# Optimization experiments

Hardware: AMD Instinct MI355X
Metric: run time of the kernel (lower is better)

The kernel has to match this reference:

```python
import jax, jax.numpy as jnp
import numpy as np

LN_EPS = 1e-5

def _layer_norm(x, gamma, beta):
    mu = jnp.mean(x, axis=-1, keepdims=True)
    var = jnp.mean(jnp.square(x - mu), axis=-1, keepdims=True)
    return (x - mu) * jax.lax.rsqrt(var + LN_EPS) * gamma + beta

def setup_inputs() -> dict:
    key = jax.random.key(0)
    ks = jax.random.split(key, 6)
    B, Lc, S, H = 8, 16384, 2048, 256
    char_embeddings = jax.random.normal(ks[0], (B, Lc, H), dtype=jnp.float32)
    # include some negative indices (-1, -2) to exercise the no-token mask path
    token_alignment = jax.random.randint(ks[1], (B, Lc), -2, S, dtype=jnp.int32).astype(jnp.int64)
    decoder_hidden_states = jax.random.normal(ks[2], (B, S, H), dtype=jnp.float32)
    scale1 = 1.0 / np.sqrt(2 * H)
    W1 = jax.random.normal(ks[3], (2 * H, H), dtype=jnp.float32) * scale1
    b1 = jnp.zeros((H,), dtype=jnp.float32)
    W2 = jax.random.normal(ks[4], (2 * H, H), dtype=jnp.float32) * scale1
    b2 = jnp.zeros((H,), dtype=jnp.float32)
    ln_gamma = jnp.ones((H,), dtype=jnp.float32)
    ln_beta = jnp.zeros((H,), dtype=jnp.float32)
    return {
        "char_embeddings": char_embeddings,
        "token_alignment": token_alignment,
        "decoder_hidden_states": decoder_hidden_states,
        "W1": W1, "b1": b1, "W2": W2, "b2": b2,
        "ln_gamma": ln_gamma, "ln_beta": ln_beta,
    }

def reference(char_embeddings, token_alignment, decoder_hidden_states,
              W1, b1, W2, b2, ln_gamma, ln_beta):
    B, Lc, H = char_embeddings.shape
    S = decoder_hidden_states.shape[1]
    # per-character gather of decoder token representations (vectorized over batch)
    valid_idx = jnp.clip(token_alignment, 0, S - 1)                         # [B, Lc]
    tok_reprs = jnp.take_along_axis(decoder_hidden_states,
                                    valid_idx[..., None].astype(jnp.int32),
                                    axis=1)                                  # [B, Lc, H]
    tok_reprs = jnp.where((token_alignment < 0)[..., None], 0.0, tok_reprs)
    # alignment_network: Linear(2H -> H)
    combined = jnp.concatenate([char_embeddings, tok_reprs], axis=-1)        # [B, Lc, 2H]
    aligned = jnp.einsum('blk,kh->blh', combined, W1) + b1                   # [B, Lc, H]
    # syllable_feature_extractor: Linear(2H->H) + LayerNorm + GELU (+ eval-mode Dropout)
    combined2 = jnp.concatenate([char_embeddings, aligned], axis=-1)         # [B, Lc, 2H]
    feats = jnp.einsum('blk,kh->blh', combined2, W2) + b2
    feats = _layer_norm(feats, ln_gamma, ln_beta)
    feats = jax.nn.gelu(feats, approximate=False)                            # torch nn.GELU exact
    return char_embeddings + feats
```

## Files before the change

kernel.cpp:

```cpp
#include <hip/hip_runtime.h>
#include <hip/hip_bf16.h>
#include <math.h>
#include <stdint.h>

#define H     256
#define K2    512
#define SDEC  2048
#define LCSH  14
#define BM    64
#define BK    64
#define NTHR  256

typedef __attribute__((ext_vector_type(8))) short  short8;
typedef __attribute__((ext_vector_type(4))) float  f32x4;

__device__ __forceinline__ unsigned short f2bf(float f) {
  union { float f; unsigned int u; } c; c.f = f;
  unsigned int u = c.u;
  unsigned int r = u + 0x7fffu + ((u >> 16) & 1u);
  return (unsigned short)(r >> 16);
}

__global__ __launch_bounds__(256) void fuse_weights(
    const float* __restrict__ W1, const float* __restrict__ W2,
    const float* __restrict__ b1, const float* __restrict__ b2,
    unsigned short* __restrict__ wft, float* __restrict__ biasf) {
  if (blockIdx.x == 32) {
    const int n = threadIdx.x;
    float a0 = b2[n], a1 = 0.f, a2 = 0.f, a3 = 0.f;
#pragma unroll 4
    for (int j = 0; j < H; j += 4) {
      a0 += b1[j + 0] * W2[(size_t)(H + j + 0) * H + n];
      a1 += b1[j + 1] * W2[(size_t)(H + j + 1) * H + n];
      a2 += b1[j + 2] * W2[(size_t)(H + j + 2) * H + n];
      a3 += b1[j + 3] * W2[(size_t)(H + j + 3) * H + n];
    }
    biasf[n] = (a0 + a1) + (a2 + a3);
    return;
  }

  __shared__ float As[64][65];
  __shared__ float Bs[64][65];
  const int t  = threadIdx.x;
  const int k0 = (blockIdx.x >> 2) * 64;
  const int n0 = (blockIdx.x & 3) * 64;
  const int lr = t >> 2;
  const int ls = t & 3;
  const int tk = t >> 4;
  const int tn = t & 15;

  float acc[4][4];
#pragma unroll
  for (int i = 0; i < 4; ++i)
#pragma unroll
    for (int c = 0; c < 4; ++c) acc[i][c] = 0.0f;

  for (int jt = 0; jt < 4; ++jt) {
    const int j0 = jt * 64;
    __syncthreads();
    const float* a_src = W1 + (size_t)(k0 + lr) * H + j0 + ls * 16;
    const float* b_src = W2 + (size_t)(H + j0 + lr) * H + n0 + ls * 16;
#pragma unroll
    for (int i = 0; i < 16; ++i) {
      As[lr][ls * 16 + i] = a_src[i];
      Bs[lr][ls * 16 + i] = b_src[i];
    }
    __syncthreads();
#pragma unroll 8
    for (int j = 0; j < 64; ++j) {
      float a[4], b[4];
#pragma unroll
      for (int i = 0; i < 4; ++i) a[i] = As[tk * 4 + i][j];
#pragma unroll
      for (int c = 0; c < 4; ++c) b[c] = Bs[j][tn * 4 + c];
#pragma unroll
      for (int i = 0; i < 4; ++i)
#pragma unroll
        for (int c = 0; c < 4; ++c) acc[i][c] += a[i] * b[c];
    }
  }

#pragma unroll
  for (int i = 0; i < 4; ++i) {
    const int k = k0 + tk * 4 + i;
#pragma unroll
    for (int c = 0; c < 4; ++c) {
      const int n = n0 + tn * 4 + c;
      float v = acc[i][c];
      if (k < H) v += W2[(size_t)k * H + n];
      wft[(size_t)n * K2 + k] = f2bf(v);
    }
  }
}

__global__ __launch_bounds__(NTHR, 3) void syl_main(
    const float* __restrict__ cemb, const int* __restrict__ tal,
    const float* __restrict__ dec, const unsigned short* __restrict__ wft,
    const float* __restrict__ biasf, const float* __restrict__ gamma,
    const float* __restrict__ beta, float* __restrict__ out) {

  __shared__ __align__(16) char smem[16640];
  unsigned short* AshC = (unsigned short*)smem;
  float* Ef = (float*)smem;

  __shared__ int   idxs[BM];
  __shared__ float msks[BM];
  __shared__ float stats[4][BM][2];

  const int t    = threadIdx.x;
  const int wave = t >> 6;
  const int lane = t & 63;
  const int quad = lane >> 4;
  const int l15  = lane & 15;

  const int nwg  = gridDim.x;
  const int bid  = ((nwg & 7) == 0)
                     ? (int)((blockIdx.x & 7) * (nwg >> 3) + (blockIdx.x >> 3))
                     : (int)blockIdx.x;
  const int row0 = bid * BM;
  const int bidx = row0 >> LCSH;
  const float* decb = dec + (size_t)bidx * SDEC * H;

  if (t < BM) {
    int ix = tal[row0 + t];
    idxs[t] = ix < 0 ? 0 : (ix >= SDEC ? SDEC - 1 : ix);
    msks[t] = ix < 0 ? 0.0f : 1.0f;
  }

  f32x4 acc[4][4];
#pragma unroll
  for (int m = 0; m < 4; ++m)
#pragma unroll
    for (int n = 0; n < 4; ++n) acc[m][n] = (f32x4){0.f, 0.f, 0.f, 0.f};

  const int srow = t >> 2;
  const int sseg = t & 3;
  const int ksS  = sseg >> 1;
  const int qS   = (sseg & 1) * 2;
  const int mS   = srow >> 4;
  const int l15S = srow & 15;
  const int wchunk0 = (ksS * 4 + mS) * 64 + qS * 16 + l15S;

  const float* arow_c = cemb + (size_t)(row0 + srow) * H + sseg * 16;

  {
    float4 f[4];
#pragma unroll
    for (int q = 0; q < 4; ++q) f[q] = *(const float4*)(arow_c + q * 4);
    unsigned short hb[16];
#pragma unroll
    for (int q = 0; q < 4; ++q) {
      hb[q * 4 + 0] = f2bf(f[q].x); hb[q * 4 + 1] = f2bf(f[q].y);
      hb[q * 4 + 2] = f2bf(f[q].z); hb[q * 4 + 3] = f2bf(f[q].w);
    }
    *(short8*)(AshC + (size_t)wchunk0 * 8)        = *(short8*)&hb[0];
    *(short8*)(AshC + (size_t)(wchunk0 + 16) * 8) = *(short8*)&hb[8];
  }
  __syncthreads();

  const int   myidx = idxs[srow];
  const float mymsk = msks[srow];
  const float* arow_d = decb + (size_t)myidx * H + sseg * 16;

  float4 pf[2][4];
#pragma unroll
  for (int q = 0; q < 4; ++q) pf[1][q] = *(const float4*)(arow_c + BK + q * 4);

#pragma unroll
  for (int ki = 0; ki < 8; ++ki) {
    const int k0 = ki * BK;
    const int buf = ki & 1;

    short8 bf[2][4];
#pragma unroll
    for (int ks = 0; ks < 2; ++ks)
#pragma unroll
      for (int n = 0; n < 4; ++n) {
        const unsigned short* bp =
            wft + (size_t)(wave * 64 + n * 16 + l15) * K2 + k0 + ks * 32 + quad * 8;
        bf[ks][n] = *(const short8*)bp;
      }

    if (ki < 6) {
      const int kt = k0 + 2 * BK;
      const float* src = (kt < H) ? (arow_c + kt) : (arow_d + (kt - H));
#pragma unroll
      for (int q = 0; q < 4; ++q) pf[ki & 1][q] = *(const float4*)(src + q * 4);
    }

#pragma unroll
    for (int ks = 0; ks < 2; ++ks) {
      short8 af[4];
#pragma unroll
      for (int m = 0; m < 4; ++m)
        af[m] = *(const short8*)(AshC +
                 (size_t)(((buf * 2 + ks) * 4 + m) * 64 + lane) * 8);
#pragma unroll
      for (int n = 0; n < 4; ++n)
#pragma unroll
        for (int m = 0; m < 4; ++m)
          acc[m][n] = __builtin_amdgcn_mfma_f32_16x16x32_bf16(
              af[m], bf[ks][n], acc[m][n], 0, 0, 0);
    }

    if (ki < 7) {
      const float sc = ((k0 + BK) >= H) ? mymsk : 1.0f;
      const float4* fw = pf[(ki + 1) & 1];
      unsigned short hb[16];
#pragma unroll
      for (int q = 0; q < 4; ++q) {
        hb[q * 4 + 0] = f2bf(fw[q].x * sc); hb[q * 4 + 1] = f2bf(fw[q].y * sc);
        hb[q * 4 + 2] = f2bf(fw[q].z * sc); hb[q * 4 + 3] = f2bf(fw[q].w * sc);
      }
      const int nb = buf ^ 1;
      *(short8*)(AshC + (size_t)(nb * 512 + wchunk0) * 8)      = *(short8*)&hb[0];
      *(short8*)(AshC + (size_t)(nb * 512 + wchunk0 + 16) * 8) = *(short8*)&hb[8];
      __syncthreads();
    }
  }

  float bvals[4], gvals[4], betv[4];
#pragma unroll
  for (int n = 0; n < 4; ++n) {
    const int col = wave * 64 + n * 16 + l15;
    bvals[n] = biasf[col];
    gvals[n] = gamma[col];
    betv[n]  = beta[col];
  }
#pragma unroll
  for (int m = 0; m < 4; ++m)
#pragma unroll
    for (int n = 0; n < 4; ++n)
#pragma unroll
      for (int r = 0; r < 4; ++r) acc[m][n][r] += bvals[n];

#pragma unroll
  for (int m = 0; m < 4; ++m)
#pragma unroll
    for (int r = 0; r < 4; ++r) {
      float a = 0.f, b = 0.f;
#pragma unroll
      for (int n = 0; n < 4; ++n) {
        const float v = acc[m][n][r];
        a += v; b += v * v;
      }
#pragma unroll
      for (int d = 1; d < 16; d <<= 1) {
        a += __shfl_xor(a, d, 64);
        b += __shfl_xor(b, d, 64);
      }
      if (l15 == 0) {
        const int row = m * 16 + quad * 4 + r;
        stats[wave][row][0] = a;
        stats[wave][row][1] = b;
      }
    }
  __syncthreads();

  float mean_[4][4], rstd_[4][4];
#pragma unroll
  for (int m = 0; m < 4; ++m)
#pragma unroll
    for (int r = 0; r < 4; ++r) {
      const int row = m * 16 + quad * 4 + r;
      const float a = stats[0][row][0] + stats[1][row][0] +
                      stats[2][row][0] + stats[3][row][0];
      const float b = stats[0][row][1] + stats[1][row][1] +
                      stats[2][row][1] + stats[3][row][1];
      const float mu  = a * (1.0f / 256.0f);
      const float var = b * (1.0f / 256.0f) - mu * mu;
      mean_[m][r] = mu;
      rstd_[m][r] = rsqrtf(var + 1e-5f);
    }

  const int erow = t >> 4;
  const int eseg = t & 15;
#pragma unroll
  for (int m = 0; m < 4; ++m) {
#pragma unroll
    for (int r = 0; r < 4; ++r) {
#pragma unroll
      for (int n = 0; n < 4; ++n) {
        const float x = (acc[m][n][r] - mean_[m][r]) * rstd_[m][r];
        const float y = x * gvals[n] + betv[n];
        const float g = 0.5f * y * (1.0f + erff(y * 0.70710678118654752f));
        Ef[(quad * 4 + r) * 260 + wave * 64 + n * 16 + l15] = g;
      }
    }
    __syncthreads();
    {
      const size_t grow = (size_t)row0 + m * 16 + erow;
      const float* crow = cemb + grow * H + eseg * 16;
      float* orow = out + grow * H + eseg * 16;
#pragma unroll
      for (int j = 0; j < 4; ++j) {
        float4 v = *(const float4*)&Ef[erow * 260 + eseg * 16 + j * 4];
        float4 c = *(const float4*)(crow + j * 4);
        v.x += c.x; v.y += c.y; v.z += c.z; v.w += c.w;
        *(float4*)(orow + j * 4) = v;
      }
    }
    __syncthreads();
  }
}

extern "C" void kernel_launch(void* const* d_in, const int* in_sizes, int n_in,
                              void* d_out, int out_size, void* d_ws, size_t ws_size,
                              hipStream_t stream) {
  const float* cemb  = (const float*)d_in[0];
  const int*   tal   = (const int*)d_in[1];
  const float* dec   = (const float*)d_in[2];
  const float* W1    = (const float*)d_in[3];
  const float* b1    = (const float*)d_in[4];
  const float* W2    = (const float*)d_in[5];
  const float* b2    = (const float*)d_in[6];
  const float* gamma = (const float*)d_in[7];
  const float* beta  = (const float*)d_in[8];
  float* out = (float*)d_out;

  unsigned short* wft = (unsigned short*)d_ws;
  float* biasf = (float*)((char*)d_ws + (size_t)K2 * H * sizeof(unsigned short));

  const int rows = in_sizes[0] / H;

  hipLaunchKernelGGL(fuse_weights, dim3(33), dim3(256), 0, stream,
                     W1, W2, b1, b2, wft, biasf);
  hipLaunchKernelGGL(syl_main, dim3(rows / BM), dim3(NTHR), 0, stream,
                     cemb, tal, dec, wft, biasf, gamma, beta, out);
}
```

Before: 405.6 us.

## Drop shared-memory staging; each wave owns 16 rows and all 256 columns

Rewrites the main kernel so each wave computes a 16-row by 256-column tile entirely in registers. A operands are loaded from global memory, converted to bf16 and fed straight into MFMA, with no LDS double buffering or block barriers. LayerNorm statistics reduce inside the wave, and the epilogue writes output directly instead of transposing through LDS. The aim is to remove synchronisation and LDS traffic. In exchange each wave now streams the whole weight matrix, raising weight bandwidth demand fourfold, and the strided output stores (16-column stride) are poorly coalesced.

```diff
diff --git a/kernel.cpp b/kernel.cpp
--- a/kernel.cpp
+++ b/kernel.cpp
@@ -8,7 +8,6 @@
 #define SDEC  2048
 #define LCSH  14
 #define BM    64
-#define BK    64
 #define NTHR  256
 
 typedef __attribute__((ext_vector_type(8))) short  short8;
@@ -99,18 +98,10 @@
     const float* __restrict__ biasf, const float* __restrict__ gamma,
     const float* __restrict__ beta, float* __restrict__ out) {
 
-  __shared__ __align__(16) char smem[16640];
-  unsigned short* AshC = (unsigned short*)smem;
-  float* Ef = (float*)smem;
-
-  __shared__ int   idxs[BM];
-  __shared__ float msks[BM];
-  __shared__ float stats[4][BM][2];
-
   const int t    = threadIdx.x;
   const int wave = t >> 6;
   const int lane = t & 63;
-  const int quad = lane >> 4;
+  const int q    = lane >> 4;
   const int l15  = lane & 15;
 
   const int nwg  = gridDim.x;
@@ -119,188 +110,104 @@
                      : (int)blockIdx.x;
   const int row0 = bid * BM;
   const int bidx = row0 >> LCSH;
-  const float* decb = dec + (size_t)bidx * SDEC * H;
-
-  if (t < BM) {
-    int ix = tal[row0 + t];
-    idxs[t] = ix < 0 ? 0 : (ix >= SDEC ? SDEC - 1 : ix);
-    msks[t] = ix < 0 ? 0.0f : 1.0f;
-  }
-
-  f32x4 acc[4][4];
-#pragma unroll
-  for (int m = 0; m < 4; ++m)
-#pragma unroll
-    for (int n = 0; n < 4; ++n) acc[m][n] = (f32x4){0.f, 0.f, 0.f, 0.f};
-
-  const int srow = t >> 2;
-  const int sseg = t & 3;
-  const int ksS  = sseg >> 1;
-  const int qS   = (sseg & 1) * 2;
-  const int mS   = srow >> 4;
-  const int l15S = srow & 15;
-  const int wchunk0 = (ksS * 4 + mS) * 64 + qS * 16 + l15S;
-
-  const float* arow_c = cemb + (size_t)(row0 + srow) * H + sseg * 16;
-
-  {
-    float4 f[4];
-#pragma unroll
-    for (int q = 0; q < 4; ++q) f[q] = *(const float4*)(arow_c + q * 4);
-    unsigned short hb[16];
-#pragma unroll
-    for (int q = 0; q < 4; ++q) {
-      hb[q * 4 + 0] = f2bf(f[q].x); hb[q * 4 + 1] = f2bf(f[q].y);
-      hb[q * 4 + 2] = f2bf(f[q].z); hb[q * 4 + 3] = f2bf(f[q].w);
-    }
-    *(short8*)(AshC + (size_t)wchunk0 * 8)        = *(short8*)&hb[0];
-    *(short8*)(AshC + (size_t)(wchunk0 + 16) * 8) = *(short8*)&hb[8];
-  }
-  __syncthreads();
-
-  const int   myidx = idxs[srow];
-  const float mymsk = msks[srow];
-  const float* arow_d = decb + (size_t)myidx * H + sseg * 16;
-
-  float4 pf[2][4];
-#pragma unroll
-  for (int q = 0; q < 4; ++q) pf[1][q] = *(const float4*)(arow_c + BK + q * 4);
-
-#pragma unroll
-  for (int ki = 0; ki < 8; ++ki) {
-    const int k0 = ki * BK;
-    const int buf = ki & 1;
-
-    short8 bf[2][4];
-#pragma unroll
-    for (int ks = 0; ks < 2; ++ks)
-#pragma unroll
-      for (int n = 0; n < 4; ++n) {
-        const unsigned short* bp =
-            wft + (size_t)(wave * 64 + n * 16 + l15) * K2 + k0 + ks * 32 + quad * 8;
-        bf[ks][n] = *(const short8*)bp;
-      }
-
-    if (ki < 6) {
-      const int kt = k0 + 2 * BK;
-      const float* src = (kt < H) ? (arow_c + kt) : (arow_d + (kt - H));
-#pragma unroll
-      for (int q = 0; q < 4; ++q) pf[ki & 1][q] = *(const float4*)(src + q * 4);
-    }
-
-#pragma unroll
-    for (int ks = 0; ks < 2; ++ks) {
-      short8 af[4];
-#pragma unroll
-      for (int m = 0; m < 4; ++m)
-        af[m] = *(const short8*)(AshC +
-                 (size_t)(((buf * 2 + ks) * 4 + m) * 64 + lane) * 8);
-#pragma unroll
-      for (int n = 0; n < 4; ++n)
-#pragma unroll
-        for (int m = 0; m < 4; ++m)
-          acc[m][n] = __builtin_amdgcn_mfma_f32_16x16x32_bf16(
-              af[m], bf[ks][n], acc[m][n], 0, 0, 0);
-    }
-
-    if (ki < 7) {
-      const float sc = ((k0 + BK) >= H) ? mymsk : 1.0f;
-      const float4* fw = pf[(ki + 1) & 1];
-      unsigned short hb[16];
-#pragma unroll
-      for (int q = 0; q < 4; ++q) {
-        hb[q * 4 + 0] = f2bf(fw[q].x * sc); hb[q * 4 + 1] = f2bf(fw[q].y * sc);
-        hb[q * 4 + 2] = f2bf(fw[q].z * sc); hb[q * 4 + 3] = f2bf(fw[q].w * sc);
-      }
-      const int nb = buf ^ 1;
-      *(short8*)(AshC + (size_t)(nb * 512 + wchunk0) * 8)      = *(short8*)&hb[0];
-      *(short8*)(AshC + (size_t)(nb * 512 + wchunk0 + 16) * 8) = *(short8*)&hb[8];
-      __syncthreads();
-    }
-  }
-
-  float bvals[4], gvals[4], betv[4];
-#pragma unroll
-  for (int n = 0; n < 4; ++n) {
-    const int col = wave * 64 + n * 16 + l15;
-    bvals[n] = biasf[col];
-    gvals[n] = gamma[col];
-    betv[n]  = beta[col];
-  }
-#pragma unroll
-  for (int m = 0; m < 4; ++m)
-#pragma unroll
-    for (int n = 0; n < 4; ++n)
-#pragma unroll
-      for (int r = 0; r < 4; ++r) acc[m][n][r] += bvals[n];
-
-#pragma unroll
-  for (int m = 0; m < 4; ++m)
-#pragma unroll
-    for (int r = 0; r < 4; ++r) {
-      float a = 0.f, b = 0.f;
-#pragma unroll
-      for (int n = 0; n < 4; ++n) {
-        const float v = acc[m][n][r];
-        a += v; b += v * v;
-      }
-#pragma unroll
-      for (int d = 1; d < 16; d <<= 1) {
-        a += __shfl_xor(a, d, 64);
-        b += __shfl_xor(b, d, 64);
-      }
-      if (l15 == 0) {
-        const int row = m * 16 + quad * 4 + r;
-        stats[wave][row][0] = a;
-        stats[wave][row][1] = b;
-      }
-    }
-  __syncthreads();
-
-  float mean_[4][4], rstd_[4][4];
-#pragma unroll
-  for (int m = 0; m < 4; ++m)
-#pragma unroll
-    for (int r = 0; r < 4; ++r) {
-      const int row = m * 16 + quad * 4 + r;
-      const float a = stats[0][row][0] + stats[1][row][0] +
-                      stats[2][row][0] + stats[3][row][0];
-      const float b = stats[0][row][1] + stats[1][row][1] +
-                      stats[2][row][1] + stats[3][row][1];
-      const float mu  = a * (1.0f / 256.0f);
-      const float var = b * (1.0f / 256.0f) - mu * mu;
-      mean_[m][r] = mu;
-      rstd_[m][r] = rsqrtf(var + 1e-5f);
-    }
-
-  const int erow = t >> 4;
-  const int eseg = t & 15;
-#pragma unroll
-  for (int m = 0; m < 4; ++m) {
-#pragma unroll
-    for (int r = 0; r < 4; ++r) {
-#pragma unroll
-      for (int n = 0; n < 4; ++n) {
-        const float x = (acc[m][n][r] - mean_[m][r]) * rstd_[m][r];
-        const float y = x * gvals[n] + betv[n];
-        const float g = 0.5f * y * (1.0f + erff(y * 0.70710678118654752f));
-        Ef[(quad * 4 + r) * 260 + wave * 64 + n * 16 + l15] = g;
-      }
-    }
-    __syncthreads();
-    {
-      const size_t grow = (size_t)row0 + m * 16 + erow;
-      const float* crow = cemb + grow * H + eseg * 16;
-      float* orow = out + grow * H + eseg * 16;
-#pragma unroll
-      for (int j = 0; j < 4; ++j) {
-        float4 v = *(const float4*)&Ef[erow * 260 + eseg * 16 + j * 4];
-        float4 c = *(const float4*)(crow + j * 4);
-        v.x += c.x; v.y += c.y; v.z += c.z; v.w += c.w;
-        *(float4*)(orow + j * 4) = v;
-      }
-    }
-    __syncthreads();
+
+  const int arow = row0 + wave * 16 + l15;
+  int ix = tal[arow];
+  const float msk = (ix < 0) ? 0.0f : 1.0f;
+  ix = ix < 0 ? 0 : (ix >= SDEC ? SDEC - 1 : ix);
+
+  const float* __restrict__ ap = cemb + (size_t)arow * H + q * 8;
+  const float* __restrict__ dp = dec + ((size_t)bidx * SDEC + ix) * H + q * 8;
+  const unsigned short* __restrict__ wp = wft + (size_t)l15 * K2 + q * 8;
+
+  f32x4 acc[16];
+#pragma unroll
+  for (int n = 0; n < 16; ++n) acc[n] = (f32x4){0.f, 0.f, 0.f, 0.f};
+
+#pragma unroll 2
+  for (int kk = 0; kk < 8; ++kk) {
+    const float4 a0 = *(const float4*)(ap + kk * 32);
+    const float4 a1 = *(const float4*)(ap + kk * 32 + 4);
+    unsigned short hb[8];
+    hb[0] = f2bf(a0.x); hb[1] = f2bf(a0.y); hb[2] = f2bf(a0.z); hb[3] = f2bf(a0.w);
+    hb[4] = f2bf(a1.x); hb[5] = f2bf(a1.y); hb[6] = f2bf(a1.z); hb[7] = f2bf(a1.w);
+    const short8 af = *(const short8*)hb;
+#pragma unroll
+    for (int h = 0; h < 2; ++h) {
+      short8 bf[8];
+#pragma unroll
+      for (int n = 0; n < 8; ++n)
+        bf[n] = *(const short8*)(wp + (size_t)((h * 8 + n) * 16) * K2 + kk * 32);
+#pragma unroll
+      for (int n = 0; n < 8; ++n)
+        acc[h * 8 + n] = __builtin_amdgcn_mfma_f32_16x16x32_bf16(
+            af, bf[n], acc[h * 8 + n], 0, 0, 0);
+    }
+  }
+
+#pragma unroll 2
+  for (int kk = 0; kk < 8; ++kk) {
+    float4 a0 = *(const float4*)(dp + kk * 32);
+    float4 a1 = *(const float4*)(dp + kk * 32 + 4);
+    a0.x *= msk; a0.y *= msk; a0.z *= msk; a0.w *= msk;
+    a1.x *= msk; a1.y *= msk; a1.z *= msk; a1.w *= msk;
+    unsigned short hb[8];
+    hb[0] = f2bf(a0.x); hb[1] = f2bf(a0.y); hb[2] = f2bf(a0.z); hb[3] = f2bf(a0.w);
+    hb[4] = f2bf(a1.x); hb[5] = f2bf(a1.y); hb[6] = f2bf(a1.z); hb[7] = f2bf(a1.w);
+    const short8 af = *(const short8*)hb;
+#pragma unroll
+    for (int h = 0; h < 2; ++h) {
+      short8 bf[8];
+#pragma unroll
+      for (int n = 0; n < 8; ++n)
+        bf[n] = *(const short8*)(wp + (size_t)((h * 8 + n) * 16) * K2 + (kk + 8) * 32);
+#pragma unroll
+      for (int n = 0; n < 8; ++n)
+        acc[h * 8 + n] = __builtin_amdgcn_mfma_f32_16x16x32_bf16(
+            af, bf[n], acc[h * 8 + n], 0, 0, 0);
+    }
+  }
+
+  float bv[16], gv[16], bev[16];
+#pragma unroll
+  for (int n = 0; n < 16; ++n) {
+    bv[n]  = biasf[n * 16 + l15];
+    gv[n]  = gamma[n * 16 + l15];
+    bev[n] = beta [n * 16 + l15];
+  }
+
+#pragma unroll
+  for (int r = 0; r < 4; ++r) {
+    float a = 0.f, b2s = 0.f;
+#pragma unroll
+    for (int n = 0; n < 16; ++n) {
+      const float v = acc[n][r] + bv[n];
+      acc[n][r] = v;
+      a += v; b2s += v * v;
+    }
+#pragma unroll
+    for (int d = 1; d < 16; d <<= 1) {
+      a   += __shfl_xor(a, d, 64);
+      b2s += __shfl_xor(b2s, d, 64);
+    }
+    const float mu   = a * (1.0f / 256.0f);
+    const float var  = b2s * (1.0f / 256.0f) - mu * mu;
+    const float rstd = rsqrtf(var + 1e-5f);
+
+    const size_t ro = ((size_t)row0 + wave * 16 + q * 4 + r) * H + l15;
+    const float* __restrict__ cr = cemb + ro;
+    float* __restrict__ orow = out + ro;
+
+    float res[16];
+#pragma unroll
+    for (int n = 0; n < 16; ++n) res[n] = cr[n * 16];
+#pragma unroll
+    for (int n = 0; n < 16; ++n) {
+      const float x = (acc[n][r] - mu) * rstd;
+      const float y = x * gv[n] + bev[n];
+      const float g = 0.5f * y * (1.0f + erff(y * 0.70710678118654752f));
+      orow[n * 16] = res[n] + g;
+    }
   }
 }
 
```

Result: slower. 504.3 us (+24.3%).
